# Kernel optimization log

Hardware: AMD Instinct MI355X
Metric: run time of the kernel (lower is better)

The kernel has to match this reference:

```python
import jax, jax.numpy as jnp
import numpy as np

K = 6                 # color-coding parameter; K-1 message-passing steps
N = 50000             # num nodes
E = 1600000           # num edges (avg degree 32)
F = 384               # num_node_features = K * 2**K


def setup_inputs() -> dict:
    key = jax.random.key(0)
    k1, k2, k3, k4, k5 = jax.random.split(key, 5)
    s = 1.0 / np.sqrt(F)
    x = jax.random.normal(k1, (N, F), dtype=jnp.float32)
    edge_index = jax.random.randint(k2, (2, E), 0, N, dtype=jnp.int32)
    batch = jnp.zeros((N,), dtype=jnp.int32)  # unused by forward, kept for signature parity
    W_rel = jax.random.normal(k3, (F, F), dtype=jnp.float32) * s   # GraphConv lin_rel weight
    W_root = jax.random.normal(k4, (F, F), dtype=jnp.float32) * s  # GraphConv lin_root weight
    W_lin = jax.random.normal(k5, (1, F), dtype=jnp.float32) * s   # readout linear (no bias)
    return {"x": x, "edge_index": edge_index, "batch": batch,
            "W_rel": W_rel, "W_root": W_root, "W_lin": W_lin}


def reference(x, edge_index, batch, W_rel, W_root, W_lin):
    src = edge_index[0]
    dst = edge_index[1]
    # K-1 iterations of PyG GraphConv(aggr='add', bias=False) + relu:
    #   out = segment_sum(x[src] -> dst) @ W_rel^T + x @ W_root^T
    for _ in range(K - 1):
        agg = jax.ops.segment_sum(x[src], dst, num_segments=N)  # [N, F]
        x = jax.nn.relu(agg @ W_rel.T + x @ W_root.T)
    # readout: Linear(F, 1, bias=False)
    return x @ W_lin.T  # [N, 1]
```

## Files before the change

kernel.cpp:

```cpp
#include <hip/hip_runtime.h>
#include <hip/hip_bf16.h>

#define NN 50000
#define EE 1600000
#define FF 384
#define MPAD 50048
#define NITER 5

typedef unsigned int u32;
typedef unsigned short u16;
typedef __attribute__((ext_vector_type(8))) short short8;
typedef __attribute__((ext_vector_type(4))) float f32x4;

typedef const __attribute__((address_space(1))) void* gptr_t;
typedef __attribute__((address_space(3))) void* lptr_t;

__device__ __forceinline__ float bf_lo(u32 u) {
  u32 v = u << 16;
  return __builtin_bit_cast(float, v);
}
__device__ __forceinline__ float bf_hi(u32 u) {
  u32 v = u & 0xFFFF0000u;
  return __builtin_bit_cast(float, v);
}
__device__ __forceinline__ u32 f2bf(float f) {
  u32 u = __builtin_bit_cast(u32, f);
  return (u + 0x7FFFu + ((u >> 16) & 1u)) >> 16;
}
__device__ __forceinline__ u32 pack2(float lo, float hi) {
  return f2bf(lo) | (f2bf(hi) << 16);
}
__device__ __forceinline__ void load16_lds(const void* g, void* l) {
  __builtin_amdgcn_global_load_lds((gptr_t)g, (lptr_t)l, 16, 0, 0);
}

__global__ void hist_kernel(const int* __restrict__ dst, int* __restrict__ cnt) {
  int e = blockIdx.x * 256 + threadIdx.x;
  if (e < EE) atomicAdd(&cnt[dst[e]], 1);
}

__global__ void scan_kernel(const int* __restrict__ cnt, int* __restrict__ row_start,
                            int* __restrict__ cursor) {
  __shared__ int wsum[4];
  const int CH = 196;
  int t = threadIdx.x;
  int lo = t * CH;
  int hi = lo + CH; if (hi > NN) hi = NN;
  int s = 0;
  int n4 = (hi - lo) >> 2;
  const int4* p = (const int4*)(cnt + lo);
  for (int i = 0; i < n4; ++i) { int4 c = p[i]; s += c.x + c.y + c.z + c.w; }
  int lane = t & 63, w = t >> 6;
  int v = s;
  for (int d = 1; d < 64; d <<= 1) { int u = __shfl_up(v, d, 64); if (lane >= d) v += u; }
  if (lane == 63) wsum[w] = v;
  __syncthreads();
  int run = v - s;
  for (int i = 0; i < w; ++i) run += wsum[i];
  int4* q1 = (int4*)(row_start + lo);
  int4* q2 = (int4*)(cursor + lo);
  for (int k = 0; k < n4; ++k) {
    int4 c = p[k];
    int4 o; o.x = run; o.y = run + c.x; o.z = o.y + c.y; o.w = o.z + c.z;
    run = o.w + c.w;
    q1[k] = o; q2[k] = o;
  }
  if (hi == NN && lo < NN) row_start[NN] = run;
}

__global__ void scatter_kernel(const int* __restrict__ src, const int* __restrict__ dst,
                               int* __restrict__ cursor, int* __restrict__ col) {
  int e = blockIdx.x * 256 + threadIdx.x;
  if (e < EE) {
    int d = dst[e];
    int p = atomicAdd(&cursor[d], 1);
    col[p] = src[e];
  }
}

__global__ void convert_x_kernel(const float* __restrict__ xin, u16* __restrict__ xout) {
  size_t i = ((size_t)blockIdx.x * 256 + threadIdx.x) * 4;
  if (i >= (size_t)NN * FF) return;
  float4 f = *(const float4*)(xin + i);
  u32 o0 = pack2(f.x, f.y);
  u32 o1 = pack2(f.z, f.w);
  u32* q = (u32*)(xout + i);
  q[0] = o0; q[1] = o1;
}

__global__ void build_bt_kernel(const float* __restrict__ Wr, const float* __restrict__ Wt,
                                u16* __restrict__ Bt) {
  int i = blockIdx.x * 256 + threadIdx.x;
  if (i >= FF * 2 * FF) return;
  int n = i / (2 * FF);
  int k = i - n * (2 * FF);
  float v = (k < FF) ? Wr[n * FF + k] : Wt[n * FF + (k - FF)];
  Bt[i] = (u16)f2bf(v);
}

#define ACC8(u)                                  \
  a0 += bf_lo(u.x); a1 += bf_hi(u.x);            \
  a2 += bf_lo(u.y); a3 += bf_hi(u.y);            \
  a4 += bf_lo(u.z); a5 += bf_hi(u.z);            \
  a6 += bf_lo(u.w); a7 += bf_hi(u.w);

__global__ void spmm_kernel(const u16* __restrict__ x, const int* __restrict__ rs,
                            const int* __restrict__ col, u16* __restrict__ agg) {
  int row = blockIdx.x * 4 + (threadIdx.x >> 6);
  int lane = threadIdx.x & 63;
  if (row >= NN) return;
  int j0 = rs[row], j1 = rs[row + 1];
  float a0 = 0.f, a1 = 0.f, a2 = 0.f, a3 = 0.f;
  float a4 = 0.f, a5 = 0.f, a6 = 0.f, a7 = 0.f;
  const bool active = lane < 48;
  const int off = lane * 4;
  int j = j0;
  for (; j + 4 <= j1; j += 4) {
    int s0 = col[j], s1 = col[j + 1], s2 = col[j + 2], s3 = col[j + 3];
    if (active) {
      uint4 u0 = *(const uint4*)((const u32*)(x + (size_t)s0 * FF) + off);
      uint4 u1 = *(const uint4*)((const u32*)(x + (size_t)s1 * FF) + off);
      uint4 u2 = *(const uint4*)((const u32*)(x + (size_t)s2 * FF) + off);
      uint4 u3 = *(const uint4*)((const u32*)(x + (size_t)s3 * FF) + off);
      ACC8(u0); ACC8(u1); ACC8(u2); ACC8(u3);
    }
  }
  for (; j < j1; ++j) {
    int s0 = col[j];
    if (active) {
      uint4 u0 = *(const uint4*)((const u32*)(x + (size_t)s0 * FF) + off);
      ACC8(u0);
    }
  }
  if (active) {
    uint4 o;
    o.x = pack2(a0, a1); o.y = pack2(a2, a3);
    o.z = pack2(a4, a5); o.w = pack2(a6, a7);
    *(uint4*)((u32*)(agg + (size_t)row * FF) + off) = o;
  }
}

__global__ __launch_bounds__(256) void gemm_kernel(
    const u16* __restrict__ Aagg, const u16* __restrict__ Ax,
    const u16* __restrict__ Bt, u16* __restrict__ Xout) {
  __shared__ __align__(16) u16 As[128 * 64];
  __shared__ __align__(16) u16 Bs[128 * 64];
  const int m0 = blockIdx.y * 128;
  const int n0 = blockIdx.x * 128;
  const int tid = threadIdx.x;
  const int lane = tid & 63;
  const int w = tid >> 6;
  const int wr = w >> 1, wc = w & 1;

  const int sr = lane >> 3;
  const int sbc = (lane & 7) << 4;

  f32x4 acc[4][4] = {};

  for (int kt = 0; kt < 12; ++kt) {
    const u16* Asrc = (kt < 6) ? Aagg : Ax;
    const int kbA = (kt < 6 ? kt : kt - 6) << 7;
    const int kbB = kt << 7;
#pragma unroll
    for (int i = 0; i < 4; ++i) {
      const int r = w * 32 + i * 8 + sr;
      const int swz = sbc ^ ((r & 7) << 4);
      load16_lds((const char*)Asrc + (size_t)(m0 + r) * 768 + kbA + swz,
                 &As[(w * 32 + i * 8) * 64]);
      load16_lds((const char*)Bt + (size_t)(n0 + r) * 1536 + kbB + swz,
                 &Bs[(w * 32 + i * 8) * 64]);
    }
    __syncthreads();
#pragma unroll
    for (int ks = 0; ks < 2; ++ks) {
      short8 af[4], bfm[4];
#pragma unroll
      for (int mi = 0; mi < 4; ++mi) {
        const int r = wr * 64 + mi * 16 + (lane & 15);
        const int bc = (ks * 64 + ((lane >> 4) << 4)) ^ ((r & 7) << 4);
        af[mi] = *(const short8*)((const char*)As + r * 128 + bc);
      }
#pragma unroll
      for (int ni = 0; ni < 4; ++ni) {
        const int r = wc * 64 + ni * 16 + (lane & 15);
        const int bc = (ks * 64 + ((lane >> 4) << 4)) ^ ((r & 7) << 4);
        bfm[ni] = *(const short8*)((const char*)Bs + r * 128 + bc);
      }
#pragma unroll
      for (int mi = 0; mi < 4; ++mi)
#pragma unroll
        for (int ni = 0; ni < 4; ++ni)
          acc[mi][ni] = __builtin_amdgcn_mfma_f32_16x16x32_bf16(af[mi], bfm[ni], acc[mi][ni], 0, 0, 0);
    }
    __syncthreads();
  }

#pragma unroll
  for (int mi = 0; mi < 4; ++mi) {
#pragma unroll
    for (int r = 0; r < 4; ++r) {
      const int row = m0 + wr * 64 + mi * 16 + ((lane >> 4) << 2) + r;
      u16* orow = Xout + (size_t)row * FF + n0 + wc * 64 + (lane & 15);
#pragma unroll
      for (int ni = 0; ni < 4; ++ni) {
        float v = fmaxf(acc[mi][ni][r], 0.0f);
        orow[ni * 16] = (u16)f2bf(v);
      }
    }
  }
}

__global__ void readout_kernel(const u16* __restrict__ x, const float* __restrict__ wl,
                               float* __restrict__ out) {
  int row = blockIdx.x * 4 + (threadIdx.x >> 6);
  int lane = threadIdx.x & 63;
  if (row >= NN) return;
  const u32* p = (const u32*)(x + (size_t)row * FF) + lane * 3;
  u32 u0 = p[0], u1 = p[1], u2 = p[2];
  const float* w = wl + lane * 6;
  float s = bf_lo(u0) * w[0] + bf_hi(u0) * w[1] +
            bf_lo(u1) * w[2] + bf_hi(u1) * w[3] +
            bf_lo(u2) * w[4] + bf_hi(u2) * w[5];
#pragma unroll
  for (int off = 32; off > 0; off >>= 1) s += __shfl_down(s, off, 64);
  if (lane == 0) out[row] = s;
}

extern "C" void kernel_launch(void* const* d_in, const int* in_sizes, int n_in,
                              void* d_out, int out_size, void* d_ws, size_t ws_size,
                              hipStream_t stream) {
  const float* x_in = (const float*)d_in[0];
  const int* ei = (const int*)d_in[1];
  const float* W_rel = (const float*)d_in[3];
  const float* W_root = (const float*)d_in[4];
  const float* W_lin = (const float*)d_in[5];
  float* out = (float*)d_out;

  char* ws = (char*)d_ws;
  int* cnt = (int*)(ws);
  int* row_start = (int*)(ws + 200064);
  int* cursor = (int*)(ws + 400128);
  int* col = (int*)(ws + 600192);
  u16* Bt = (u16*)(ws + 7000192);
  u16* agg = (u16*)(ws + 7590016);
  u16* x0 = (u16*)(ws + 46026880);
  u16* x1 = (u16*)(ws + 84463744);
  if (ws_size < (size_t)122900608) return;

  const int* esrc = ei;
  const int* edst = ei + EE;

  hipMemsetAsync(cnt, 0, NN * sizeof(int), stream);
  hipMemsetAsync(agg + (size_t)NN * FF, 0, (size_t)(MPAD - NN) * FF * sizeof(u16), stream);
  hipMemsetAsync(x0 + (size_t)NN * FF, 0, (size_t)(MPAD - NN) * FF * sizeof(u16), stream);
  hipMemsetAsync(x1 + (size_t)NN * FF, 0, (size_t)(MPAD - NN) * FF * sizeof(u16), stream);

  hist_kernel<<<EE / 256, 256, 0, stream>>>(edst, cnt);
  scan_kernel<<<1, 256, 0, stream>>>(cnt, row_start, cursor);
  scatter_kernel<<<EE / 256, 256, 0, stream>>>(esrc, edst, cursor, col);
  convert_x_kernel<<<(NN * FF / 4 + 255) / 256, 256, 0, stream>>>(x_in, x0);
  build_bt_kernel<<<(FF * 2 * FF + 255) / 256, 256, 0, stream>>>(W_rel, W_root, Bt);

  u16* xs = x0;
  u16* xd = x1;
  for (int t = 0; t < NITER; ++t) {
    spmm_kernel<<<NN / 4, 256, 0, stream>>>(xs, row_start, col, agg);
    gemm_kernel<<<dim3(FF / 128, MPAD / 128), 256, 0, stream>>>(agg, xs, Bt, xd);
    u16* tmp = xs; xs = xd; xd = tmp;
  }
  readout_kernel<<<NN / 4, 256, 0, stream>>>(xs, W_lin, out);
}
```

Measured before the change: 1.321 ms.

## Double-buffer GEMM LDS, remap blocks per XCD, use all lanes in SpMM

The GEMM now uses two LDS buffers so the next K-tile's global-to-LDS loads are issued while the current tile is multiplied, removing one barrier per iteration. Blocks are launched on a 1D grid and remapped so that consecutive workgroups on the same XCD share A rows, which is meant to improve L2 reuse. The SpMM kernel switches from 48 active lanes with 16-byte loads to all 64 lanes with 12-byte loads, so no lanes sit idle, at the cost of loads that are no longer 16-byte aligned. LDS use doubles, which may reduce occupancy.

```diff
diff --git a/kernel.cpp b/kernel.cpp
--- a/kernel.cpp
+++ b/kernel.cpp
@@ -34,9 +34,9 @@
   __builtin_amdgcn_global_load_lds((gptr_t)g, (lptr_t)l, 16, 0, 0);
 }
 
-__global__ void hist_kernel(const int* __restrict__ dst, int* __restrict__ cnt) {
+__global__ void hist_kernel(const int* __restrict__ key, int* __restrict__ cnt) {
   int e = blockIdx.x * 256 + threadIdx.x;
-  if (e < EE) atomicAdd(&cnt[dst[e]], 1);
+  if (e < EE) atomicAdd(&cnt[key[e]], 1);
 }
 
 __global__ void scan_kernel(const int* __restrict__ cnt, int* __restrict__ row_start,
@@ -98,11 +98,11 @@
   Bt[i] = (u16)f2bf(v);
 }
 
-#define ACC8(u)                                  \
+struct u32x3 { u32 x, y, z; };
+#define ACC6(u)                                  \
   a0 += bf_lo(u.x); a1 += bf_hi(u.x);            \
   a2 += bf_lo(u.y); a3 += bf_hi(u.y);            \
-  a4 += bf_lo(u.z); a5 += bf_hi(u.z);            \
-  a6 += bf_lo(u.w); a7 += bf_hi(u.w);
+  a4 += bf_lo(u.z); a5 += bf_hi(u.z);
 
 __global__ void spmm_kernel(const u16* __restrict__ x, const int* __restrict__ rs,
                             const int* __restrict__ col, u16* __restrict__ agg) {
@@ -110,43 +110,41 @@
   int lane = threadIdx.x & 63;
   if (row >= NN) return;
   int j0 = rs[row], j1 = rs[row + 1];
-  float a0 = 0.f, a1 = 0.f, a2 = 0.f, a3 = 0.f;
-  float a4 = 0.f, a5 = 0.f, a6 = 0.f, a7 = 0.f;
-  const bool active = lane < 48;
-  const int off = lane * 4;
+  float a0 = 0.f, a1 = 0.f, a2 = 0.f, a3 = 0.f, a4 = 0.f, a5 = 0.f;
+  const int off = lane * 3;
   int j = j0;
   for (; j + 4 <= j1; j += 4) {
     int s0 = col[j], s1 = col[j + 1], s2 = col[j + 2], s3 = col[j + 3];
-    if (active) {
-      uint4 u0 = *(const uint4*)((const u32*)(x + (size_t)s0 * FF) + off);
-      uint4 u1 = *(const uint4*)((const u32*)(x + (size_t)s1 * FF) + off);
-      uint4 u2 = *(const uint4*)((const u32*)(x + (size_t)s2 * FF) + off);
-      uint4 u3 = *(const uint4*)((const u32*)(x + (size_t)s3 * FF) + off);
-      ACC8(u0); ACC8(u1); ACC8(u2); ACC8(u3);
-    }
+    u32x3 u0 = *(const u32x3*)((const u32*)(x + (size_t)s0 * FF) + off);
+    u32x3 u1 = *(const u32x3*)((const u32*)(x + (size_t)s1 * FF) + off);
+    u32x3 u2 = *(const u32x3*)((const u32*)(x + (size_t)s2 * FF) + off);
+    u32x3 u3 = *(const u32x3*)((const u32*)(x + (size_t)s3 * FF) + off);
+    ACC6(u0); ACC6(u1); ACC6(u2); ACC6(u3);
   }
   for (; j < j1; ++j) {
     int s0 = col[j];
-    if (active) {
-      uint4 u0 = *(const uint4*)((const u32*)(x + (size_t)s0 * FF) + off);
-      ACC8(u0);
-    }
-  }
-  if (active) {
-    uint4 o;
-    o.x = pack2(a0, a1); o.y = pack2(a2, a3);
-    o.z = pack2(a4, a5); o.w = pack2(a6, a7);
-    *(uint4*)((u32*)(agg + (size_t)row * FF) + off) = o;
-  }
+    u32x3 u0 = *(const u32x3*)((const u32*)(x + (size_t)s0 * FF) + off);
+    ACC6(u0);
+  }
+  u32* q = (u32*)(agg + (size_t)row * FF) + off;
+  q[0] = pack2(a0, a1);
+  q[1] = pack2(a2, a3);
+  q[2] = pack2(a4, a5);
 }
 
 __global__ __launch_bounds__(256) void gemm_kernel(
     const u16* __restrict__ Aagg, const u16* __restrict__ Ax,
     const u16* __restrict__ Bt, u16* __restrict__ Xout) {
-  __shared__ __align__(16) u16 As[128 * 64];
-  __shared__ __align__(16) u16 Bs[128 * 64];
-  const int m0 = blockIdx.y * 128;
-  const int n0 = blockIdx.x * 128;
+  __shared__ __align__(16) u16 As[2][128 * 64];
+  __shared__ __align__(16) u16 Bs[2][128 * 64];
+
+  const int orig = blockIdx.x;
+  const int xcd = orig & 7, idx = orig >> 3;
+  const int base = (xcd < 5) ? xcd * 147 : 5 * 147 + (xcd - 5) * 146;
+  const int wg = base + idx;
+  const int m0 = (wg / 3) * 128;
+  const int n0 = (wg % 3) * 128;
+
   const int tid = threadIdx.x;
   const int lane = tid & 63;
   const int w = tid >> 6;
@@ -157,20 +155,28 @@
 
   f32x4 acc[4][4] = {};
 
+#define STAGE(KT, BUF)                                                          \
+  {                                                                             \
+    const u16* Asrc_ = ((KT) < 6) ? Aagg : Ax;                                  \
+    const int kbA_ = (((KT) < 6) ? (KT) : (KT)-6) << 7;                         \
+    const int kbB_ = (KT) << 7;                                                 \
+    _Pragma("unroll")                                                           \
+    for (int i = 0; i < 4; ++i) {                                               \
+      const int r = w * 32 + i * 8 + sr;                                        \
+      const int swz = sbc ^ ((r & 7) << 4);                                     \
+      load16_lds((const char*)Asrc_ + (size_t)(m0 + r) * 768 + kbA_ + swz,      \
+                 &As[BUF][(w * 32 + i * 8) * 64]);                              \
+      load16_lds((const char*)Bt + (size_t)(n0 + r) * 1536 + kbB_ + swz,        \
+                 &Bs[BUF][(w * 32 + i * 8) * 64]);                              \
+    }                                                                           \
+  }
+
+  STAGE(0, 0);
+  __syncthreads();
+
+  int buf = 0;
   for (int kt = 0; kt < 12; ++kt) {
-    const u16* Asrc = (kt < 6) ? Aagg : Ax;
-    const int kbA = (kt < 6 ? kt : kt - 6) << 7;
-    const int kbB = kt << 7;
-#pragma unroll
-    for (int i = 0; i < 4; ++i) {
-      const int r = w * 32 + i * 8 + sr;
-      const int swz = sbc ^ ((r & 7) << 4);
-      load16_lds((const char*)Asrc + (size_t)(m0 + r) * 768 + kbA + swz,
-                 &As[(w * 32 + i * 8) * 64]);
-      load16_lds((const char*)Bt + (size_t)(n0 + r) * 1536 + kbB + swz,
-                 &Bs[(w * 32 + i * 8) * 64]);
-    }
-    __syncthreads();
+    if (kt < 11) STAGE(kt + 1, buf ^ 1);
 #pragma unroll
     for (int ks = 0; ks < 2; ++ks) {
       short8 af[4], bfm[4];
@@ -178,13 +184,13 @@
       for (int mi = 0; mi < 4; ++mi) {
         const int r = wr * 64 + mi * 16 + (lane & 15);
         const int bc = (ks * 64 + ((lane >> 4) << 4)) ^ ((r & 7) << 4);
-        af[mi] = *(const short8*)((const char*)As + r * 128 + bc);
+        af[mi] = *(const short8*)((const char*)&As[buf][0] + r * 128 + bc);
       }
 #pragma unroll
       for (int ni = 0; ni < 4; ++ni) {
         const int r = wc * 64 + ni * 16 + (lane & 15);
         const int bc = (ks * 64 + ((lane >> 4) << 4)) ^ ((r & 7) << 4);
-        bfm[ni] = *(const short8*)((const char*)Bs + r * 128 + bc);
+        bfm[ni] = *(const short8*)((const char*)&Bs[buf][0] + r * 128 + bc);
       }
 #pragma unroll
       for (int mi = 0; mi < 4; ++mi)
@@ -193,6 +199,7 @@
           acc[mi][ni] = __builtin_amdgcn_mfma_f32_16x16x32_bf16(af[mi], bfm[ni], acc[mi][ni], 0, 0, 0);
     }
     __syncthreads();
+    buf ^= 1;
   }
 
 #pragma unroll
@@ -208,6 +215,7 @@
       }
     }
   }
+#undef STAGE
 }
 
 __global__ void readout_kernel(const u16* __restrict__ x, const float* __restrict__ wl,
@@ -265,7 +273,7 @@
   u16* xd = x1;
   for (int t = 0; t < NITER; ++t) {
     spmm_kernel<<<NN / 4, 256, 0, stream>>>(xs, row_start, col, agg);
-    gemm_kernel<<<dim3(FF / 128, MPAD / 128), 256, 0, stream>>>(agg, xs, Bt, xd);
+    gemm_kernel<<<(MPAD / 128) * (FF / 128), 256, 0, stream>>>(agg, xs, Bt, xd);
     u16* tmp = xs; xs = xd; xd = tmp;
   }
   readout_kernel<<<NN / 4, 256, 0, stream>>>(xs, W_lin, out);
```

Result: faster. 1.291 ms (-2.2%).
